# Kernel optimization log

Hardware: AMD Instinct MI355X
Metric: run time of the kernel (lower is better)

Reference implementation:

```python
import jax, jax.numpy as jnp
import numpy as np

D_MODEL = 256
NUM_HEADS = 4
EPS = 1e-6


def setup_inputs() -> dict:
    key = jax.random.key(0)
    ks = jax.random.split(key, 9)
    B, T, D = 4, 2048, D_MODEL
    scale = 1.0 / np.sqrt(D)
    inp = {
        "x": jax.random.normal(ks[0], (B, T, D), dtype=jnp.float32),
        "Wq": jax.random.normal(ks[1], (D, D), dtype=jnp.float32) * scale,
        "bq": jnp.zeros((D,), dtype=jnp.float32),
        "Wk": jax.random.normal(ks[2], (D, D), dtype=jnp.float32) * scale,
        "bk": jnp.zeros((D,), dtype=jnp.float32),
        "Wv": jax.random.normal(ks[3], (D, D), dtype=jnp.float32) * scale,
        "bv": jnp.zeros((D,), dtype=jnp.float32),
        "Wo": jax.random.normal(ks[4], (D, D), dtype=jnp.float32) * scale,
        "bo": jnp.zeros((D,), dtype=jnp.float32),
    }
    return inp


def _feature_map(a):
    # F.elu(x) + 1.0
    return jax.nn.elu(a) + 1.0


def reference(x, Wq, bq, Wk, bk, Wv, bv, Wo, bo):
    B, T, D = x.shape
    H = NUM_HEADS
    dh = D // H
    Q = _feature_map((x @ Wq + bq).reshape(B, T, H, dh))
    K = _feature_map((x @ Wk + bk).reshape(B, T, H, dh))
    V = (x @ Wv + bv).reshape(B, T, H, dh)
    # outer-product state: (B,T,H,dh,dh), cumulative over time
    KV = jnp.einsum('bthd,bthm->bthdm', K, V)
    S = jnp.cumsum(KV, axis=1)
    Z = jnp.cumsum(K, axis=1)
    out = jnp.einsum('bthd,bthdm->bthm', Q, S)
    denom = jnp.einsum('bthd,bthd->bth', Q, Z)[..., None] + EPS
    out = (out / denom).reshape(B, T, D)
    return out @ Wo + bo
```

## Files before the change

### kernel.cpp

```cpp
#include <hip/hip_runtime.h>
#include <hip/hip_bf16.h>

#define D_MODEL 256
#define NHEADS 4
#define DHEAD 64
#define BATCH 4
#define TSEQ 2048
#define CHUNK 64
#define NCHUNK (TSEQ / CHUNK)
#define NTOK (BATCH * TSEQ)
#define NBH (BATCH * NHEADS)
#define EPSV 1e-6f
#define LSTRF 68
#define PQ 36

typedef __bf16 bf16x8 __attribute__((ext_vector_type(8)));
typedef float f32x4 __attribute__((ext_vector_type(4)));
typedef unsigned short us8 __attribute__((ext_vector_type(8)));

__device__ __forceinline__ float elu1(float a) {
    return a > 0.0f ? a + 1.0f : __expf(a);
}

__device__ __forceinline__ unsigned short f2bf(float f) {
    __hip_bfloat16 h = __float2bfloat16(f);
    return __builtin_bit_cast(unsigned short, h);
}

__device__ __forceinline__ float bf2f(unsigned short u) {
    return __bfloat162float(__builtin_bit_cast(__hip_bfloat16, u));
}

__device__ __forceinline__ void unpack2(unsigned int u, float& lo, float& hi) {
    lo = __builtin_bit_cast(float, u << 16);
    hi = __builtin_bit_cast(float, u & 0xFFFF0000u);
}

__device__ __forceinline__ bf16x8 frag8(const float* p) {
    const float4 x = *reinterpret_cast<const float4*>(p);
    const float4 y = *reinterpret_cast<const float4*>(p + 4);
    us8 u;
    u[0] = f2bf(x.x); u[1] = f2bf(x.y); u[2] = f2bf(x.z); u[3] = f2bf(x.w);
    u[4] = f2bf(y.x); u[5] = f2bf(y.y); u[6] = f2bf(y.z); u[7] = f2bf(y.w);
    return __builtin_bit_cast(bf16x8, u);
}

__device__ __forceinline__ void gld_lds16(const void* g, void* l) {
    __builtin_amdgcn_global_load_lds(
        (const __attribute__((address_space(1))) void*)g,
        (__attribute__((address_space(3))) void*)l, 16, 0, 0);
}

__global__ __launch_bounds__(256) void convert_kernel(
    const float* __restrict__ x,
    const float* __restrict__ Wq, const float* __restrict__ Wk,
    const float* __restrict__ Wv, const float* __restrict__ Wo,
    unsigned short* __restrict__ xb,
    unsigned short* __restrict__ Wt, unsigned short* __restrict__ Wot)
{
    const int tid = threadIdx.x;
    if (blockIdx.x < NTOK * D_MODEL / 8 / 256) {
        const int i = (blockIdx.x * 256 + tid) * 8;
        const float4 a = *reinterpret_cast<const float4*>(&x[i]);
        const float4 b = *reinterpret_cast<const float4*>(&x[i + 4]);
        ushort4 u0 = { f2bf(a.x), f2bf(a.y), f2bf(a.z), f2bf(a.w) };
        ushort4 u1 = { f2bf(b.x), f2bf(b.y), f2bf(b.z), f2bf(b.w) };
        *reinterpret_cast<ushort4*>(&xb[i]) = u0;
        *reinterpret_cast<ushort4*>(&xb[i + 4]) = u1;
        return;
    }
    __shared__ float Ls[64][65];
    const int bid = blockIdx.x - NTOK * D_MODEL / 8 / 256;
    const int wi = bid >> 4;
    const int ti = bid & 15;
    const int k0 = (ti >> 2) * 64, n0 = (ti & 3) * 64;
    const float* W = wi == 0 ? Wq : wi == 1 ? Wk : wi == 2 ? Wv : Wo;
#pragma unroll
    for (int i = 0; i < 16; ++i) {
        const int idx = i * 256 + tid;
        const int r = idx >> 6, c = idx & 63;
        Ls[r][c] = W[(size_t)(k0 + r) * D_MODEL + n0 + c];
    }
    __syncthreads();
    unsigned short* outp = (wi < 3) ? (Wt + (size_t)(wi * 256 + n0) * D_MODEL + k0)
                                    : (Wot + (size_t)n0 * D_MODEL + k0);
#pragma unroll
    for (int i = 0; i < 16; ++i) {
        const int idx = i * 256 + tid;
        const int rn = idx >> 6, ck = idx & 63;
        outp[(size_t)rn * D_MODEL + ck] = f2bf(Ls[ck][rn]);
    }
}

template<int MODE>
__global__ __launch_bounds__(256) void mfma_gemm_kernel(
    const unsigned short* __restrict__ A,
    const unsigned short* __restrict__ Bt,
    const float* __restrict__ b0, const float* __restrict__ b1,
    const float* __restrict__ b2,
    void* __restrict__ O0, void* __restrict__ O1, void* __restrict__ O2)
{
    __shared__ __align__(16) unsigned short As[64 * 64];
    __shared__ __align__(16) unsigned short Bs[64 * 64];
    const int tid = threadIdx.x;
    const int wave = tid >> 6, lane = tid & 63;
    const int la = lane & 15, q = lane >> 4;

    int mtile, ntile;
    if (MODE == 0) { ntile = blockIdx.x % 12; mtile = blockIdx.x / 12; }
    else           { ntile = blockIdx.x & 3;  mtile = blockIdx.x >> 2; }
    const int m0 = mtile * 64, n0 = ntile * 64;

    const unsigned short* Ab = A  + (size_t)m0 * D_MODEL;
    const unsigned short* Bb = Bt + (size_t)n0 * D_MODEL;

    f32x4 acc[4];
#pragma unroll
    for (int i = 0; i < 4; ++i) acc[i] = (f32x4){0.f, 0.f, 0.f, 0.f};

    for (int k0 = 0; k0 < D_MODEL; k0 += 64) {
#pragma unroll
        for (int i = 0; i < 2; ++i) {
            const int bslot = i * 256 + wave * 64;
            const int slot = bslot + lane;
            const int m = slot >> 3, s = slot & 7;
            const int g = s ^ (m & 7);
            gld_lds16(Ab + (size_t)m * D_MODEL + k0 + g * 8, &As[bslot * 8]);
            gld_lds16(Bb + (size_t)m * D_MODEL + k0 + g * 8, &Bs[bslot * 8]);
        }
        __syncthreads();

        bf16x8 af[2], bfr[4][2];
#pragma unroll
        for (int kh = 0; kh < 2; ++kh) {
            const int g = kh * 4 + q;
            const int m = wave * 16 + la;
            af[kh] = *reinterpret_cast<const bf16x8*>(
                &As[m * 64 + ((g ^ (m & 7)) << 3)]);
#pragma unroll
            for (int ni = 0; ni < 4; ++ni) {
                const int n = ni * 16 + la;
                bfr[ni][kh] = *reinterpret_cast<const bf16x8*>(
                    &Bs[n * 64 + ((g ^ (n & 7)) << 3)]);
            }
        }
#pragma unroll
        for (int ni = 0; ni < 4; ++ni) {
            acc[ni] = __builtin_amdgcn_mfma_f32_16x16x32_bf16(
                af[0], bfr[ni][0], acc[ni], 0, 0, 0);
            acc[ni] = __builtin_amdgcn_mfma_f32_16x16x32_bf16(
                af[1], bfr[ni][1], acc[ni], 0, 0, 0);
        }
        __syncthreads();
    }

#pragma unroll
    for (int ni = 0; ni < 4; ++ni) {
        const int row = m0 + wave * 16 + q * 4;
        const int col = n0 + ni * 16 + la;
        if (MODE == 0) {
            const int which = col >> 8;
            const int cl = col & 255;
            unsigned short* Out = (unsigned short*)
                (which == 0 ? O0 : which == 1 ? O1 : O2);
            const float* bias = which == 0 ? b0 : which == 1 ? b1 : b2;
            const int act = (which < 2);
            const float bv = bias[cl];
#pragma unroll
            for (int r = 0; r < 4; ++r) {
                float v = acc[ni][r] + bv;
                if (act) v = elu1(v);
                Out[(size_t)(row + r) * D_MODEL + cl] = f2bf(v);
            }
        } else {
            float* Out = (float*)O0;
            const float bv = b0[col];
#pragma unroll
            for (int r = 0; r < 4; ++r)
                Out[(size_t)(row + r) * D_MODEL + col] = acc[ni][r] + bv;
        }
    }
}

__global__ __launch_bounds__(256) void chunksum_kernel(
    const unsigned short* __restrict__ Kb, const unsigned short* __restrict__ Vb,
    unsigned short* __restrict__ Pb16, float* __restrict__ Zc)
{
    __shared__ __align__(16) unsigned int Ktp[DHEAD * PQ];
    __shared__ __align__(16) unsigned int Vtp[DHEAD * PQ];
    const int tid = threadIdx.x;
    const int c  = blockIdx.x % NCHUNK;
    const int bh = blockIdx.x / NCHUNK;
    const int b = bh / NHEADS, h = bh % NHEADS;
    const size_t gbase = ((size_t)(b * TSEQ + c * CHUNK)) * D_MODEL + h * DHEAD;

    {
        const int sp = tid & 31, mg = tid >> 5;
        const int e0 = mg * 8;
        const uint4 k0 = *reinterpret_cast<const uint4*>(
            &Kb[gbase + (size_t)(2 * sp) * D_MODEL + e0]);
        const uint4 k1 = *reinterpret_cast<const uint4*>(
            &Kb[gbase + (size_t)(2 * sp + 1) * D_MODEL + e0]);
        const uint4 v0 = *reinterpret_cast<const uint4*>(
            &Vb[gbase + (size_t)(2 * sp) * D_MODEL + e0]);
        const uint4 v1 = *reinterpret_cast<const uint4*>(
            &Vb[gbase + (size_t)(2 * sp + 1) * D_MODEL + e0]);
        const unsigned short* ke = reinterpret_cast<const unsigned short*>(&k0);
        const unsigned short* ko2 = reinterpret_cast<const unsigned short*>(&k1);
        const unsigned short* ve = reinterpret_cast<const unsigned short*>(&v0);
        const unsigned short* vo = reinterpret_cast<const unsigned short*>(&v1);
#pragma unroll
        for (int j = 0; j < 8; ++j) {
            Ktp[(e0 + j) * PQ + sp] =
                (unsigned int)ke[j] | ((unsigned int)ko2[j] << 16);
            Vtp[(e0 + j) * PQ + sp] =
                (unsigned int)ve[j] | ((unsigned int)vo[j] << 16);
        }
    }
    __syncthreads();

    const int wave = tid >> 6, lane = tid & 63;
    const int la = lane & 15, q = lane >> 4;
    const int wm = (wave >> 1) * 32, wn = (wave & 1) * 32;

    f32x4 acc[2][2];
#pragma unroll
    for (int i = 0; i < 2; ++i)
#pragma unroll
        for (int j = 0; j < 2; ++j) acc[i][j] = (f32x4){0.f, 0.f, 0.f, 0.f};

#pragma unroll
    for (int ks = 0; ks < 2; ++ks) {
        const int ku = ks * 16 + q * 4;
        const bf16x8 a0  = __builtin_bit_cast(bf16x8,
            *reinterpret_cast<const uint4*>(&Vtp[(wm + la) * PQ + ku]));
        const bf16x8 a1  = __builtin_bit_cast(bf16x8,
            *reinterpret_cast<const uint4*>(&Vtp[(wm + 16 + la) * PQ + ku]));
        const bf16x8 bb0 = __builtin_bit_cast(bf16x8,
            *reinterpret_cast<const uint4*>(&Ktp[(wn + la) * PQ + ku]));
        const bf16x8 bb1 = __builtin_bit_cast(bf16x8,
            *reinterpret_cast<const uint4*>(&Ktp[(wn + 16 + la) * PQ + ku]));
        acc[0][0] = __builtin_amdgcn_mfma_f32_16x16x32_bf16(a0, bb0, acc[0][0], 0, 0, 0);
        acc[0][1] = __builtin_amdgcn_mfma_f32_16x16x32_bf16(a0, bb1, acc[0][1], 0, 0, 0);
        acc[1][0] = __builtin_amdgcn_mfma_f32_16x16x32_bf16(a1, bb0, acc[1][0], 0, 0, 0);
        acc[1][1] = __builtin_amdgcn_mfma_f32_16x16x32_bf16(a1, bb1, acc[1][1], 0, 0, 0);
    }

    unsigned short* Pb = Pb16 + (size_t)blockIdx.x * (DHEAD * DHEAD);
#pragma unroll
    for (int mi = 0; mi < 2; ++mi)
#pragma unroll
        for (int ni = 0; ni < 2; ++ni) {
            const int row = wm + mi * 16 + q * 4;
            const int col = wn + ni * 16 + la;
#pragma unroll
            for (int r = 0; r < 4; ++r)
                Pb[(row + r) * DHEAD + col] = f2bf(acc[mi][ni][r]);
        }

    if (tid < DHEAD) {
        float z = 0.f;
        for (int tt = 0; tt < 32; ++tt) {
            float lo, hi;
            unpack2(Ktp[tid * PQ + tt], lo, hi);
            z += lo;
            z += hi;
        }
        Zc[(size_t)blockIdx.x * DHEAD + tid] = z;
    }
}

__global__ __launch_bounds__(256) void prefix_kernel(
    const unsigned short* __restrict__ Pb16, float* __restrict__ Zc,
    unsigned short* __restrict__ Sb)
{
    const int tid = threadIdx.x;
    if (blockIdx.x < NBH * 16) {
        const int bh = blockIdx.x >> 4;
        const int e = ((blockIdx.x & 15) << 8) + tid;
        const size_t base = (size_t)bh * NCHUNK * (DHEAD * DHEAD) + e;
        float v[NCHUNK];
#pragma unroll
        for (int c = 0; c < NCHUNK; ++c)
            v[c] = bf2f(Pb16[base + (size_t)c * (DHEAD * DHEAD)]);
        float s = 0.f;
#pragma unroll
        for (int c = 0; c < NCHUNK; ++c) {
            const float t = v[c];
            Sb[base + (size_t)c * (DHEAD * DHEAD)] = f2bf(s);
            s += t;
        }
    } else {
        const int j = ((int)(blockIdx.x - NBH * 16) << 8) + tid;
        if (j < NBH * DHEAD) {
            const int bh = j >> 6, d = j & 63;
            float v[NCHUNK];
#pragma unroll
            for (int c = 0; c < NCHUNK; ++c) v[c] = Zc[(bh * NCHUNK + c) * DHEAD + d];
            float s = 0.f;
#pragma unroll
            for (int c = 0; c < NCHUNK; ++c) {
                const float t = v[c];
                Zc[(bh * NCHUNK + c) * DHEAD + d] = s;
                s += t;
            }
        }
    }
}

__global__ __launch_bounds__(256) void chunkout_kernel(
    const unsigned short* __restrict__ Qb, const unsigned short* __restrict__ Kb,
    const unsigned short* __restrict__ Vb,
    const unsigned short* __restrict__ Sb, const float* __restrict__ Zx,
    unsigned short* __restrict__ Ob)
{
    __shared__ __align__(16) unsigned int Qp[CHUNK * PQ];
    __shared__ __align__(16) unsigned int Kp[CHUNK * PQ];
    __shared__ __align__(16) unsigned int Vtp[DHEAD * PQ];
    __shared__ __align__(16) float At[CHUNK * LSTRF];
    __shared__ float zsh[DHEAD];
    __shared__ float dnm[CHUNK];

    const int tid = threadIdx.x;
    const int c  = blockIdx.x % NCHUNK;
    const int bh = blockIdx.x / NCHUNK;
    const int b = bh / NHEADS, h = bh % NHEADS;
    const size_t gbase = ((size_t)(b * TSEQ + c * CHUNK)) * D_MODEL + h * DHEAD;
    const unsigned short* Sp = Sb + (size_t)blockIdx.x * (DHEAD * DHEAD);

#pragma unroll
    for (int i = 0; i < 2; ++i) {
        const int idx = i * 256 + tid;
        const int t = idx >> 3, e4 = (idx & 7) * 4;
        const uint4 qv = *reinterpret_cast<const uint4*>(
            &Qb[gbase + (size_t)t * D_MODEL + e4 * 2]);
        const uint4 kv = *reinterpret_cast<const uint4*>(
            &Kb[gbase + (size_t)t * D_MODEL + e4 * 2]);
        *reinterpret_cast<uint4*>(&Qp[t * PQ + e4]) = qv;
        *reinterpret_cast<uint4*>(&Kp[t * PQ + e4]) = kv;
    }
    {
        const int sp = tid & 31, mg = tid >> 5;
        const int m0 = mg * 8;
        const uint4 v0 = *reinterpret_cast<const uint4*>(
            &Vb[gbase + (size_t)(2 * sp) * D_MODEL + m0]);
        const uint4 v1 = *reinterpret_cast<const uint4*>(
            &Vb[gbase + (size_t)(2 * sp + 1) * D_MODEL + m0]);
        const unsigned short* ev = reinterpret_cast<const unsigned short*>(&v0);
        const unsigned short* ov = reinterpret_cast<const unsigned short*>(&v1);
#pragma unroll
        for (int j = 0; j < 8; ++j)
            Vtp[(m0 + j) * PQ + sp] =
                (unsigned int)ev[j] | ((unsigned int)ov[j] << 16);
    }
    if (tid < DHEAD)
        zsh[tid] = Zx[((size_t)bh * NCHUNK + c) * DHEAD + tid];
    __syncthreads();

    const int wave = tid >> 6, lane = tid & 63;
    const int la = lane & 15, q = lane >> 4;
    const int wt = (wave >> 1) * 32, wn = (wave & 1) * 32;

    f32x4 acc[2][2];
#pragma unroll
    for (int i = 0; i < 2; ++i)
#pragma unroll
        for (int j = 0; j < 2; ++j) acc[i][j] = (f32x4){0.f, 0.f, 0.f, 0.f};
#pragma unroll
    for (int ks = 0; ks < 2; ++ks) {
        const int ku = ks * 16 + q * 4;
        const bf16x8 a0  = __builtin_bit_cast(bf16x8,
            *reinterpret_cast<const uint4*>(&Qp[(wt + la) * PQ + ku]));
        const bf16x8 a1  = __builtin_bit_cast(bf16x8,
            *reinterpret_cast<const uint4*>(&Qp[(wt + 16 + la) * PQ + ku]));
        const bf16x8 bb0 = __builtin_bit_cast(bf16x8,
            *reinterpret_cast<const uint4*>(&Kp[(wn + la) * PQ + ku]));
        const bf16x8 bb1 = __builtin_bit_cast(bf16x8,
            *reinterpret_cast<const uint4*>(&Kp[(wn + 16 + la) * PQ + ku]));
        acc[0][0] = __builtin_amdgcn_mfma_f32_16x16x32_bf16(a0, bb0, acc[0][0], 0, 0, 0);
        acc[0][1] = __builtin_amdgcn_mfma_f32_16x16x32_bf16(a0, bb1, acc[0][1], 0, 0, 0);
        acc[1][0] = __builtin_amdgcn_mfma_f32_16x16x32_bf16(a1, bb0, acc[1][0], 0, 0, 0);
        acc[1][1] = __builtin_amdgcn_mfma_f32_16x16x32_bf16(a1, bb1, acc[1][1], 0, 0, 0);
    }
#pragma unroll
    for (int mi = 0; mi < 2; ++mi)
#pragma unroll
        for (int ni = 0; ni < 2; ++ni) {
            const int t0 = wt + mi * 16 + q * 4;
            const int s  = wn + ni * 16 + la;
#pragma unroll
            for (int r = 0; r < 4; ++r)
                At[(t0 + r) * LSTRF + s] = (s <= t0 + r) ? acc[mi][ni][r] : 0.f;
        }
    __syncthreads();

    if (tid < CHUNK) {
        float dv = 0.f;
        for (int s = 0; s < CHUNK; ++s) dv += At[tid * LSTRF + s];
        for (int dd = 0; dd < 32; ++dd) {
            float lo, hi;
            unpack2(Qp[tid * PQ + dd], lo, hi);
            dv = fmaf(lo, zsh[2 * dd], dv);
            dv = fmaf(hi, zsh[2 * dd + 1], dv);
        }
        dnm[tid] = dv + EPSV;
    }
    __syncthreads();

    f32x4 o[2][2];
#pragma unroll
    for (int i = 0; i < 2; ++i)
#pragma unroll
        for (int j = 0; j < 2; ++j) o[i][j] = (f32x4){0.f, 0.f, 0.f, 0.f};
#pragma unroll
    for (int ks = 0; ks < 2; ++ks) {
        const int ku = ks * 16 + q * 4;
        const int ko = ks * 32 + q * 8;
        const bf16x8 a0  = __builtin_bit_cast(bf16x8,
            *reinterpret_cast<const uint4*>(&Qp[(wt + la) * PQ + ku]));
        const bf16x8 a1  = __builtin_bit_cast(bf16x8,
            *reinterpret_cast<const uint4*>(&Qp[(wt + 16 + la) * PQ + ku]));
        const bf16x8 bb0 = __builtin_bit_cast(bf16x8,
            *reinterpret_cast<const uint4*>(&Sp[(wn + la) * DHEAD + ko]));
        const bf16x8 bb1 = __builtin_bit_cast(bf16x8,
            *reinterpret_cast<const uint4*>(&Sp[(wn + 16 + la) * DHEAD + ko]));
        o[0][0] = __builtin_amdgcn_mfma_f32_16x16x32_bf16(a0, bb0, o[0][0], 0, 0, 0);
        o[0][1] = __builtin_amdgcn_mfma_f32_16x16x32_bf16(a0, bb1, o[0][1], 0, 0, 0);
        o[1][0] = __builtin_amdgcn_mfma_f32_16x16x32_bf16(a1, bb0, o[1][0], 0, 0, 0);
        o[1][1] = __builtin_amdgcn_mfma_f32_16x16x32_bf16(a1, bb1, o[1][1], 0, 0, 0);
    }
#pragma unroll
    for (int ks = 0; ks < 2; ++ks) {
        const int ku = ks * 16 + q * 4;
        const int ko = ks * 32 + q * 8;
        const bf16x8 a0  = frag8(&At[(wt + la) * LSTRF + ko]);
        const bf16x8 a1  = frag8(&At[(wt + 16 + la) * LSTRF + ko]);
        const bf16x8 bb0 = __builtin_bit_cast(bf16x8,
            *reinterpret_cast<const uint4*>(&Vtp[(wn + la) * PQ + ku]));
        const bf16x8 bb1 = __builtin_bit_cast(bf16x8,
            *reinterpret_cast<const uint4*>(&Vtp[(wn + 16 + la) * PQ + ku]));
        o[0][0] = __builtin_amdgcn_mfma_f32_16x16x32_bf16(a0, bb0, o[0][0], 0, 0, 0);
        o[0][1] = __builtin_amdgcn_mfma_f32_16x16x32_bf16(a0, bb1, o[0][1], 0, 0, 0);
        o[1][0] = __builtin_amdgcn_mfma_f32_16x16x32_bf16(a1, bb0, o[1][0], 0, 0, 0);
        o[1][1] = __builtin_amdgcn_mfma_f32_16x16x32_bf16(a1, bb1, o[1][1], 0, 0, 0);
    }

#pragma unroll
    for (int mi = 0; mi < 2; ++mi)
#pragma unroll
        for (int ni = 0; ni < 2; ++ni) {
            const int t0 = wt + mi * 16 + q * 4;
            const int m  = wn + ni * 16 + la;
#pragma unroll
            for (int r = 0; r < 4; ++r) {
                const float v = o[mi][ni][r] / dnm[t0 + r];
                Ob[gbase + (size_t)(t0 + r) * D_MODEL + m] = f2bf(v);
            }
        }
}

extern "C" void kernel_launch(void* const* d_in, const int* in_sizes, int n_in,
                              void* d_out, int out_size, void* d_ws, size_t ws_size,
                              hipStream_t stream)
{
    const float* x  = (const float*)d_in[0];
    const float* Wq = (const float*)d_in[1];
    const float* bq = (const float*)d_in[2];
    const float* Wk = (const float*)d_in[3];
    const float* bk = (const float*)d_in[4];
    const float* Wv = (const float*)d_in[5];
    const float* bv = (const float*)d_in[6];
    const float* Wo = (const float*)d_in[7];
    const float* bo = (const float*)d_in[8];
    float* out = (float*)d_out;

    const size_t NE = (size_t)NTOK * D_MODEL;
    const size_t PE = (size_t)NBH * NCHUNK * DHEAD * DHEAD;
    unsigned short* xb   = (unsigned short*)d_ws;
    unsigned short* Wt   = xb + NE;
    unsigned short* Wot  = Wt + 768 * 256;
    unsigned short* Qb   = Wot + 256 * 256;
    unsigned short* Kb   = Qb + NE;
    unsigned short* Vb   = Kb + NE;
    unsigned short* Ob   = Vb + NE;
    unsigned short* Sb   = Ob + NE;
    unsigned short* Pb16 = Sb + PE;
    float* Z = (float*)(Pb16 + PE);

    convert_kernel<<<NTOK * D_MODEL / 8 / 256 + 64, 256, 0, stream>>>(
        x, Wq, Wk, Wv, Wo, xb, Wt, Wot);
    mfma_gemm_kernel<0><<<(NTOK / 64) * 12, 256, 0, stream>>>(
        xb, Wt, bq, bk, bv, Qb, Kb, Vb);
    chunksum_kernel<<<NBH * NCHUNK, 256, 0, stream>>>(Kb, Vb, Pb16, Z);
    prefix_kernel<<<NBH * 16 + 4, 256, 0, stream>>>(Pb16, Z, Sb);
    chunkout_kernel<<<NBH * NCHUNK, 256, 0, stream>>>(Qb, Kb, Vb, Sb, Z, Ob);
    mfma_gemm_kernel<1><<<(NTOK / 64) * 4, 256, 0, stream>>>(
        Ob, Wot, bo, nullptr, nullptr, out, nullptr, nullptr);
}
```

Measured before the change: 105.1 us.

## Fuse six pipeline kernels into one cooperative kernel with grid syncs

Replaces the six separate launches (convert, QKV GEMM, chunk sums, prefix scan, chunk output, output GEMM) with one persistent cooperative kernel of 512 blocks. Phases are separated by grid.sync, and shared memory is a union reused across phases. The goal is to remove launch gaps and per-kernel ramp-up and drain. In exchange, work is fixed to 512 blocks (several tiles per block in some phases), each grid barrier costs time, and some phases leave blocks idle.

```diff
diff --git a/kernel.cpp b/kernel.cpp
--- a/kernel.cpp
+++ b/kernel.cpp
@@ -1,5 +1,8 @@
 #include <hip/hip_runtime.h>
 #include <hip/hip_bf16.h>
+#include <hip/hip_cooperative_groups.h>
+
+namespace cg = cooperative_groups;
 
 #define D_MODEL 256
 #define NHEADS 4
@@ -13,6 +16,7 @@
 #define EPSV 1e-6f
 #define LSTRF 68
 #define PQ 36
+#define NBLK 512
 
 typedef __bf16 bf16x8 __attribute__((ext_vector_type(8)));
 typedef float f32x4 __attribute__((ext_vector_type(4)));
@@ -51,65 +55,35 @@
         (__attribute__((address_space(3))) void*)l, 16, 0, 0);
 }
 
-__global__ __launch_bounds__(256) void convert_kernel(
-    const float* __restrict__ x,
-    const float* __restrict__ Wq, const float* __restrict__ Wk,
-    const float* __restrict__ Wv, const float* __restrict__ Wo,
-    unsigned short* __restrict__ xb,
-    unsigned short* __restrict__ Wt, unsigned short* __restrict__ Wot)
-{
-    const int tid = threadIdx.x;
-    if (blockIdx.x < NTOK * D_MODEL / 8 / 256) {
-        const int i = (blockIdx.x * 256 + tid) * 8;
-        const float4 a = *reinterpret_cast<const float4*>(&x[i]);
-        const float4 b = *reinterpret_cast<const float4*>(&x[i + 4]);
-        ushort4 u0 = { f2bf(a.x), f2bf(a.y), f2bf(a.z), f2bf(a.w) };
-        ushort4 u1 = { f2bf(b.x), f2bf(b.y), f2bf(b.z), f2bf(b.w) };
-        *reinterpret_cast<ushort4*>(&xb[i]) = u0;
-        *reinterpret_cast<ushort4*>(&xb[i + 4]) = u1;
-        return;
-    }
-    __shared__ float Ls[64][65];
-    const int bid = blockIdx.x - NTOK * D_MODEL / 8 / 256;
-    const int wi = bid >> 4;
-    const int ti = bid & 15;
-    const int k0 = (ti >> 2) * 64, n0 = (ti & 3) * 64;
-    const float* W = wi == 0 ? Wq : wi == 1 ? Wk : wi == 2 ? Wv : Wo;
-#pragma unroll
-    for (int i = 0; i < 16; ++i) {
-        const int idx = i * 256 + tid;
-        const int r = idx >> 6, c = idx & 63;
-        Ls[r][c] = W[(size_t)(k0 + r) * D_MODEL + n0 + c];
-    }
-    __syncthreads();
-    unsigned short* outp = (wi < 3) ? (Wt + (size_t)(wi * 256 + n0) * D_MODEL + k0)
-                                    : (Wot + (size_t)n0 * D_MODEL + k0);
-#pragma unroll
-    for (int i = 0; i < 16; ++i) {
-        const int idx = i * 256 + tid;
-        const int rn = idx >> 6, ck = idx & 63;
-        outp[(size_t)rn * D_MODEL + ck] = f2bf(Ls[ck][rn]);
-    }
-}
+struct SGemm { unsigned short As[64 * 64]; unsigned short Bs[64 * 64]; };
+struct SConv { float Ls[64][65]; };
+struct SCsum { unsigned int Ktp[DHEAD * PQ]; unsigned int Vtp[DHEAD * PQ]; };
+struct SCout {
+    unsigned int Qp[CHUNK * PQ];
+    unsigned int Kp[CHUNK * PQ];
+    unsigned int Vtp[DHEAD * PQ];
+    float At[CHUNK * LSTRF];
+    float zsh[DHEAD];
+    float dnm[CHUNK];
+};
+union SMem {
+    SGemm g;
+    SConv c;
+    SCsum s;
+    SCout o;
+};
 
 template<int MODE>
-__global__ __launch_bounds__(256) void mfma_gemm_kernel(
-    const unsigned short* __restrict__ A,
-    const unsigned short* __restrict__ Bt,
+__device__ __forceinline__ void gemm_tile(
+    int m0, int n0,
+    const unsigned short* __restrict__ A, const unsigned short* __restrict__ Bt,
     const float* __restrict__ b0, const float* __restrict__ b1,
     const float* __restrict__ b2,
-    void* __restrict__ O0, void* __restrict__ O1, void* __restrict__ O2)
+    void* __restrict__ O0, void* __restrict__ O1, void* __restrict__ O2,
+    unsigned short* As, unsigned short* Bs, int tid)
 {
-    __shared__ __align__(16) unsigned short As[64 * 64];
-    __shared__ __align__(16) unsigned short Bs[64 * 64];
-    const int tid = threadIdx.x;
     const int wave = tid >> 6, lane = tid & 63;
     const int la = lane & 15, q = lane >> 4;
-
-    int mtile, ntile;
-    if (MODE == 0) { ntile = blockIdx.x % 12; mtile = blockIdx.x / 12; }
-    else           { ntile = blockIdx.x & 3;  mtile = blockIdx.x >> 2; }
-    const int m0 = mtile * 64, n0 = ntile * 64;
 
     const unsigned short* Ab = A  + (size_t)m0 * D_MODEL;
     const unsigned short* Bb = Bt + (size_t)n0 * D_MODEL;
@@ -182,102 +156,156 @@
     }
 }
 
-__global__ __launch_bounds__(256) void chunksum_kernel(
-    const unsigned short* __restrict__ Kb, const unsigned short* __restrict__ Vb,
-    unsigned short* __restrict__ Pb16, float* __restrict__ Zc)
+__global__ __launch_bounds__(256, 2) void fused_kernel(
+    const float* __restrict__ x,
+    const float* __restrict__ Wq, const float* __restrict__ bq,
+    const float* __restrict__ Wk, const float* __restrict__ bk,
+    const float* __restrict__ Wv, const float* __restrict__ bv,
+    const float* __restrict__ Wo, const float* __restrict__ bo,
+    unsigned short* __restrict__ xb,
+    unsigned short* __restrict__ Wt, unsigned short* __restrict__ Wot,
+    unsigned short* __restrict__ Qb, unsigned short* __restrict__ Kb,
+    unsigned short* __restrict__ Vb, unsigned short* __restrict__ Ob,
+    unsigned short* __restrict__ Sb, unsigned short* __restrict__ Pb16,
+    float* __restrict__ Z, float* __restrict__ out)
 {
-    __shared__ __align__(16) unsigned int Ktp[DHEAD * PQ];
-    __shared__ __align__(16) unsigned int Vtp[DHEAD * PQ];
+    __shared__ __align__(16) SMem sm;
     const int tid = threadIdx.x;
-    const int c  = blockIdx.x % NCHUNK;
-    const int bh = blockIdx.x / NCHUNK;
-    const int b = bh / NHEADS, h = bh % NHEADS;
-    const size_t gbase = ((size_t)(b * TSEQ + c * CHUNK)) * D_MODEL + h * DHEAD;
+    const int bidx = blockIdx.x;
+    cg::grid_group grid = cg::this_grid();
 
     {
-        const int sp = tid & 31, mg = tid >> 5;
-        const int e0 = mg * 8;
-        const uint4 k0 = *reinterpret_cast<const uint4*>(
-            &Kb[gbase + (size_t)(2 * sp) * D_MODEL + e0]);
-        const uint4 k1 = *reinterpret_cast<const uint4*>(
-            &Kb[gbase + (size_t)(2 * sp + 1) * D_MODEL + e0]);
-        const uint4 v0 = *reinterpret_cast<const uint4*>(
-            &Vb[gbase + (size_t)(2 * sp) * D_MODEL + e0]);
-        const uint4 v1 = *reinterpret_cast<const uint4*>(
-            &Vb[gbase + (size_t)(2 * sp + 1) * D_MODEL + e0]);
-        const unsigned short* ke = reinterpret_cast<const unsigned short*>(&k0);
-        const unsigned short* ko2 = reinterpret_cast<const unsigned short*>(&k1);
-        const unsigned short* ve = reinterpret_cast<const unsigned short*>(&v0);
-        const unsigned short* vo = reinterpret_cast<const unsigned short*>(&v1);
-#pragma unroll
-        for (int j = 0; j < 8; ++j) {
-            Ktp[(e0 + j) * PQ + sp] =
-                (unsigned int)ke[j] | ((unsigned int)ko2[j] << 16);
-            Vtp[(e0 + j) * PQ + sp] =
-                (unsigned int)ve[j] | ((unsigned int)vo[j] << 16);
-        }
-    }
-    __syncthreads();
-
-    const int wave = tid >> 6, lane = tid & 63;
-    const int la = lane & 15, q = lane >> 4;
-    const int wm = (wave >> 1) * 32, wn = (wave & 1) * 32;
-
-    f32x4 acc[2][2];
-#pragma unroll
-    for (int i = 0; i < 2; ++i)
-#pragma unroll
-        for (int j = 0; j < 2; ++j) acc[i][j] = (f32x4){0.f, 0.f, 0.f, 0.f};
-
-#pragma unroll
-    for (int ks = 0; ks < 2; ++ks) {
-        const int ku = ks * 16 + q * 4;
-        const bf16x8 a0  = __builtin_bit_cast(bf16x8,
-            *reinterpret_cast<const uint4*>(&Vtp[(wm + la) * PQ + ku]));
-        const bf16x8 a1  = __builtin_bit_cast(bf16x8,
-            *reinterpret_cast<const uint4*>(&Vtp[(wm + 16 + la) * PQ + ku]));
-        const bf16x8 bb0 = __builtin_bit_cast(bf16x8,
-            *reinterpret_cast<const uint4*>(&Ktp[(wn + la) * PQ + ku]));
-        const bf16x8 bb1 = __builtin_bit_cast(bf16x8,
-            *reinterpret_cast<const uint4*>(&Ktp[(wn + 16 + la) * PQ + ku]));
-        acc[0][0] = __builtin_amdgcn_mfma_f32_16x16x32_bf16(a0, bb0, acc[0][0], 0, 0, 0);
-        acc[0][1] = __builtin_amdgcn_mfma_f32_16x16x32_bf16(a0, bb1, acc[0][1], 0, 0, 0);
-        acc[1][0] = __builtin_amdgcn_mfma_f32_16x16x32_bf16(a1, bb0, acc[1][0], 0, 0, 0);
-        acc[1][1] = __builtin_amdgcn_mfma_f32_16x16x32_bf16(a1, bb1, acc[1][1], 0, 0, 0);
-    }
-
-    unsigned short* Pb = Pb16 + (size_t)blockIdx.x * (DHEAD * DHEAD);
-#pragma unroll
-    for (int mi = 0; mi < 2; ++mi)
-#pragma unroll
-        for (int ni = 0; ni < 2; ++ni) {
-            const int row = wm + mi * 16 + q * 4;
-            const int col = wn + ni * 16 + la;
-#pragma unroll
-            for (int r = 0; r < 4; ++r)
-                Pb[(row + r) * DHEAD + col] = f2bf(acc[mi][ni][r]);
-        }
-
-    if (tid < DHEAD) {
-        float z = 0.f;
-        for (int tt = 0; tt < 32; ++tt) {
-            float lo, hi;
-            unpack2(Ktp[tid * PQ + tt], lo, hi);
-            z += lo;
-            z += hi;
-        }
-        Zc[(size_t)blockIdx.x * DHEAD + tid] = z;
-    }
-}
-
-__global__ __launch_bounds__(256) void prefix_kernel(
-    const unsigned short* __restrict__ Pb16, float* __restrict__ Zc,
-    unsigned short* __restrict__ Sb)
-{
-    const int tid = threadIdx.x;
-    if (blockIdx.x < NBH * 16) {
-        const int bh = blockIdx.x >> 4;
-        const int e = ((blockIdx.x & 15) << 8) + tid;
+        const int id = bidx * 256 + tid;
+#pragma unroll
+        for (int u = 0; u < 2; ++u) {
+            const int i = (id + u * (NBLK * 256)) * 8;
+            const float4 a = *reinterpret_cast<const float4*>(&x[i]);
+            const float4 b = *reinterpret_cast<const float4*>(&x[i + 4]);
+            ushort4 u0 = { f2bf(a.x), f2bf(a.y), f2bf(a.z), f2bf(a.w) };
+            ushort4 u1 = { f2bf(b.x), f2bf(b.y), f2bf(b.z), f2bf(b.w) };
+            *reinterpret_cast<ushort4*>(&xb[i]) = u0;
+            *reinterpret_cast<ushort4*>(&xb[i + 4]) = u1;
+        }
+        if (bidx < 64) {
+            const int wi = bidx >> 4;
+            const int ti = bidx & 15;
+            const int k0 = (ti >> 2) * 64, n0 = (ti & 3) * 64;
+            const float* W = wi == 0 ? Wq : wi == 1 ? Wk : wi == 2 ? Wv : Wo;
+#pragma unroll
+            for (int i = 0; i < 16; ++i) {
+                const int idx = i * 256 + tid;
+                const int r = idx >> 6, c2 = idx & 63;
+                sm.c.Ls[r][c2] = W[(size_t)(k0 + r) * D_MODEL + n0 + c2];
+            }
+            __syncthreads();
+            unsigned short* outp = (wi < 3)
+                ? (Wt + (size_t)(wi * 256 + n0) * D_MODEL + k0)
+                : (Wot + (size_t)n0 * D_MODEL + k0);
+#pragma unroll
+            for (int i = 0; i < 16; ++i) {
+                const int idx = i * 256 + tid;
+                const int rn = idx >> 6, ck = idx & 63;
+                outp[(size_t)rn * D_MODEL + ck] = f2bf(sm.c.Ls[ck][rn]);
+            }
+        }
+    }
+    grid.sync();
+
+#pragma unroll
+    for (int t = 0; t < 3; ++t) {
+        const int tile = bidx + t * NBLK;
+        const int ntile = tile % 12, mtile = tile / 12;
+        gemm_tile<0>(mtile * 64, ntile * 64, xb, Wt, bq, bk, bv,
+                     Qb, Kb, Vb, sm.g.As, sm.g.Bs, tid);
+    }
+    grid.sync();
+
+    {
+        const int c  = bidx % NCHUNK;
+        const int bh = bidx / NCHUNK;
+        const int b = bh / NHEADS, h = bh % NHEADS;
+        const size_t gbase = ((size_t)(b * TSEQ + c * CHUNK)) * D_MODEL + h * DHEAD;
+
+        {
+            const int sp = tid & 31, mg = tid >> 5;
+            const int e0 = mg * 8;
+            const uint4 k0 = *reinterpret_cast<const uint4*>(
+                &Kb[gbase + (size_t)(2 * sp) * D_MODEL + e0]);
+            const uint4 k1 = *reinterpret_cast<const uint4*>(
+                &Kb[gbase + (size_t)(2 * sp + 1) * D_MODEL + e0]);
+            const uint4 v0 = *reinterpret_cast<const uint4*>(
+                &Vb[gbase + (size_t)(2 * sp) * D_MODEL + e0]);
+            const uint4 v1 = *reinterpret_cast<const uint4*>(
+                &Vb[gbase + (size_t)(2 * sp + 1) * D_MODEL + e0]);
+            const unsigned short* ke  = reinterpret_cast<const unsigned short*>(&k0);
+            const unsigned short* ko2 = reinterpret_cast<const unsigned short*>(&k1);
+            const unsigned short* ve  = reinterpret_cast<const unsigned short*>(&v0);
+            const unsigned short* vo  = reinterpret_cast<const unsigned short*>(&v1);
+#pragma unroll
+            for (int j = 0; j < 8; ++j) {
+                sm.s.Ktp[(e0 + j) * PQ + sp] =
+                    (unsigned int)ke[j] | ((unsigned int)ko2[j] << 16);
+                sm.s.Vtp[(e0 + j) * PQ + sp] =
+                    (unsigned int)ve[j] | ((unsigned int)vo[j] << 16);
+            }
+        }
+        __syncthreads();
+
+        const int wave = tid >> 6, lane = tid & 63;
+        const int la = lane & 15, q = lane >> 4;
+        const int wm = (wave >> 1) * 32, wn = (wave & 1) * 32;
+
+        f32x4 acc[2][2];
+#pragma unroll
+        for (int i = 0; i < 2; ++i)
+#pragma unroll
+            for (int j = 0; j < 2; ++j) acc[i][j] = (f32x4){0.f, 0.f, 0.f, 0.f};
+
+#pragma unroll
+        for (int ks = 0; ks < 2; ++ks) {
+            const int ku = ks * 16 + q * 4;
+            const bf16x8 a0  = __builtin_bit_cast(bf16x8,
+                *reinterpret_cast<const uint4*>(&sm.s.Vtp[(wm + la) * PQ + ku]));
+            const bf16x8 a1  = __builtin_bit_cast(bf16x8,
+                *reinterpret_cast<const uint4*>(&sm.s.Vtp[(wm + 16 + la) * PQ + ku]));
+            const bf16x8 bb0 = __builtin_bit_cast(bf16x8,
+                *reinterpret_cast<const uint4*>(&sm.s.Ktp[(wn + la) * PQ + ku]));
+            const bf16x8 bb1 = __builtin_bit_cast(bf16x8,
+                *reinterpret_cast<const uint4*>(&sm.s.Ktp[(wn + 16 + la) * PQ + ku]));
+            acc[0][0] = __builtin_amdgcn_mfma_f32_16x16x32_bf16(a0, bb0, acc[0][0], 0, 0, 0);
+            acc[0][1] = __builtin_amdgcn_mfma_f32_16x16x32_bf16(a0, bb1, acc[0][1], 0, 0, 0);
+            acc[1][0] = __builtin_amdgcn_mfma_f32_16x16x32_bf16(a1, bb0, acc[1][0], 0, 0, 0);
+            acc[1][1] = __builtin_amdgcn_mfma_f32_16x16x32_bf16(a1, bb1, acc[1][1], 0, 0, 0);
+        }
+
+        unsigned short* Pb = Pb16 + (size_t)bidx * (DHEAD * DHEAD);
+#pragma unroll
+        for (int mi = 0; mi < 2; ++mi)
+#pragma unroll
+            for (int ni = 0; ni < 2; ++ni) {
+                const int row = wm + mi * 16 + q * 4;
+                const int col = wn + ni * 16 + la;
+#pragma unroll
+                for (int r = 0; r < 4; ++r)
+                    Pb[(row + r) * DHEAD + col] = f2bf(acc[mi][ni][r]);
+            }
+
+        if (tid < DHEAD) {
+            float z = 0.f;
+            for (int tt = 0; tt < 32; ++tt) {
+                float lo, hi;
+                unpack2(sm.s.Ktp[tid * PQ + tt], lo, hi);
+                z += lo;
+                z += hi;
+            }
+            Z[(size_t)bidx * DHEAD + tid] = z;
+        }
+    }
+    grid.sync();
+
+    if (bidx < NBH * 16) {
+        const int bh = bidx >> 4;
+        const int e = ((bidx & 15) << 8) + tid;
         const size_t base = (size_t)bh * NCHUNK * (DHEAD * DHEAD) + e;
         float v[NCHUNK];
 #pragma unroll
@@ -290,173 +318,168 @@
             Sb[base + (size_t)c * (DHEAD * DHEAD)] = f2bf(s);
             s += t;
         }
-    } else {
-        const int j = ((int)(blockIdx.x - NBH * 16) << 8) + tid;
+    } else if (bidx < NBH * 16 + 4) {
+        const int j = ((bidx - NBH * 16) << 8) + tid;
         if (j < NBH * DHEAD) {
             const int bh = j >> 6, d = j & 63;
             float v[NCHUNK];
 #pragma unroll
-            for (int c = 0; c < NCHUNK; ++c) v[c] = Zc[(bh * NCHUNK + c) * DHEAD + d];
+            for (int c = 0; c < NCHUNK; ++c) v[c] = Z[(bh * NCHUNK + c) * DHEAD + d];
             float s = 0.f;
 #pragma unroll
             for (int c = 0; c < NCHUNK; ++c) {
                 const float t = v[c];
-                Zc[(bh * NCHUNK + c) * DHEAD + d] = s;
+                Z[(bh * NCHUNK + c) * DHEAD + d] = s;
                 s += t;
             }
         }
     }
-}
-
-__global__ __launch_bounds__(256) void chunkout_kernel(
-    const unsigned short* __restrict__ Qb, const unsigned short* __restrict__ Kb,
-    const unsigned short* __restrict__ Vb,
-    const unsigned short* __restrict__ Sb, const float* __restrict__ Zx,
-    unsigned short* __restrict__ Ob)
-{
-    __shared__ __align__(16) unsigned int Qp[CHUNK * PQ];
-    __shared__ __align__(16) unsigned int Kp[CHUNK * PQ];
-    __shared__ __align__(16) unsigned int Vtp[DHEAD * PQ];
-    __shared__ __align__(16) float At[CHUNK * LSTRF];
-    __shared__ float zsh[DHEAD];
-    __shared__ float dnm[CHUNK];
-
-    const int tid = threadIdx.x;
-    const int c  = blockIdx.x % NCHUNK;
-    const int bh = blockIdx.x / NCHUNK;
-    const int b = bh / NHEADS, h = bh % NHEADS;
-    const size_t gbase = ((size_t)(b * TSEQ + c * CHUNK)) * D_MODEL + h * DHEAD;
-    const unsigned short* Sp = Sb + (size_t)blockIdx.x * (DHEAD * DHEAD);
-
-#pragma unroll
-    for (int i = 0; i < 2; ++i) {
-        const int idx = i * 256 + tid;
-        const int t = idx >> 3, e4 = (idx & 7) * 4;
-        const uint4 qv = *reinterpret_cast<const uint4*>(
-            &Qb[gbase + (size_t)t * D_MODEL + e4 * 2]);
-        const uint4 kv = *reinterpret_cast<const uint4*>(
-            &Kb[gbase + (size_t)t * D_MODEL + e4 * 2]);
-        *reinterpret_cast<uint4*>(&Qp[t * PQ + e4]) = qv;
-        *reinterpret_cast<uint4*>(&Kp[t * PQ + e4]) = kv;
-    }
+    grid.sync();
+
     {
-        const int sp = tid & 31, mg = tid >> 5;
-        const int m0 = mg * 8;
-        const uint4 v0 = *reinterpret_cast<const uint4*>(
-            &Vb[gbase + (size_t)(2 * sp) * D_MODEL + m0]);
-        const uint4 v1 = *reinterpret_cast<const uint4*>(
-            &Vb[gbase + (size_t)(2 * sp + 1) * D_MODEL + m0]);
-        const unsigned short* ev = reinterpret_cast<const unsigned short*>(&v0);
-        const unsigned short* ov = reinterpret_cast<const unsigned short*>(&v1);
-#pragma unroll
-        for (int j = 0; j < 8; ++j)
-            Vtp[(m0 + j) * PQ + sp] =
-                (unsigned int)ev[j] | ((unsigned int)ov[j] << 16);
-    }
-    if (tid < DHEAD)
-        zsh[tid] = Zx[((size_t)bh * NCHUNK + c) * DHEAD + tid];
-    __syncthreads();
-
-    const int wave = tid >> 6, lane = tid & 63;
-    const int la = lane & 15, q = lane >> 4;
-    const int wt = (wave >> 1) * 32, wn = (wave & 1) * 32;
-
-    f32x4 acc[2][2];
-#pragma unroll
-    for (int i = 0; i < 2; ++i)
-#pragma unroll
-        for (int j = 0; j < 2; ++j) acc[i][j] = (f32x4){0.f, 0.f, 0.f, 0.f};
-#pragma unroll
-    for (int ks = 0; ks < 2; ++ks) {
-        const int ku = ks * 16 + q * 4;
-        const bf16x8 a0  = __builtin_bit_cast(bf16x8,
-            *reinterpret_cast<const uint4*>(&Qp[(wt + la) * PQ + ku]));
-        const bf16x8 a1  = __builtin_bit_cast(bf16x8,
-            *reinterpret_cast<const uint4*>(&Qp[(wt + 16 + la) * PQ + ku]));
-        const bf16x8 bb0 = __builtin_bit_cast(bf16x8,
-            *reinterpret_cast<const uint4*>(&Kp[(wn + la) * PQ + ku]));
-        const bf16x8 bb1 = __builtin_bit_cast(bf16x8,
-            *reinterpret_cast<const uint4*>(&Kp[(wn + 16 + la) * PQ + ku]));
-        acc[0][0] = __builtin_amdgcn_mfma_f32_16x16x32_bf16(a0, bb0, acc[0][0], 0, 0, 0);
-        acc[0][1] = __builtin_amdgcn_mfma_f32_16x16x32_bf16(a0, bb1, acc[0][1], 0, 0, 0);
-        acc[1][0] = __builtin_amdgcn_mfma_f32_16x16x32_bf16(a1, bb0, acc[1][0], 0, 0, 0);
-        acc[1][1] = __builtin_amdgcn_mfma_f32_16x16x32_bf16(a1, bb1, acc[1][1], 0, 0, 0);
-    }
-#pragma unroll
-    for (int mi = 0; mi < 2; ++mi)
-#pragma unroll
-        for (int ni = 0; ni < 2; ++ni) {
-            const int t0 = wt + mi * 16 + q * 4;
-            const int s  = wn + ni * 16 + la;
-#pragma unroll
-            for (int r = 0; r < 4; ++r)
-                At[(t0 + r) * LSTRF + s] = (s <= t0 + r) ? acc[mi][ni][r] : 0.f;
-        }
-    __syncthreads();
-
-    if (tid < CHUNK) {
-        float dv = 0.f;
-        for (int s = 0; s < CHUNK; ++s) dv += At[tid * LSTRF + s];
-        for (int dd = 0; dd < 32; ++dd) {
-            float lo, hi;
-            unpack2(Qp[tid * PQ + dd], lo, hi);
-            dv = fmaf(lo, zsh[2 * dd], dv);
-            dv = fmaf(hi, zsh[2 * dd + 1], dv);
-        }
-        dnm[tid] = dv + EPSV;
-    }
-    __syncthreads();
-
-    f32x4 o[2][2];
-#pragma unroll
-    for (int i = 0; i < 2; ++i)
-#pragma unroll
-        for (int j = 0; j < 2; ++j) o[i][j] = (f32x4){0.f, 0.f, 0.f, 0.f};
-#pragma unroll
-    for (int ks = 0; ks < 2; ++ks) {
-        const int ku = ks * 16 + q * 4;
-        const int ko = ks * 32 + q * 8;
-        const bf16x8 a0  = __builtin_bit_cast(bf16x8,
-            *reinterpret_cast<const uint4*>(&Qp[(wt + la) * PQ + ku]));
-        const bf16x8 a1  = __builtin_bit_cast(bf16x8,
-            *reinterpret_cast<const uint4*>(&Qp[(wt + 16 + la) * PQ + ku]));
-        const bf16x8 bb0 = __builtin_bit_cast(bf16x8,
-            *reinterpret_cast<const uint4*>(&Sp[(wn + la) * DHEAD + ko]));
-        const bf16x8 bb1 = __builtin_bit_cast(bf16x8,
-            *reinterpret_cast<const uint4*>(&Sp[(wn + 16 + la) * DHEAD + ko]));
-        o[0][0] = __builtin_amdgcn_mfma_f32_16x16x32_bf16(a0, bb0, o[0][0], 0, 0, 0);
-        o[0][1] = __builtin_amdgcn_mfma_f32_16x16x32_bf16(a0, bb1, o[0][1], 0, 0, 0);
-        o[1][0] = __builtin_amdgcn_mfma_f32_16x16x32_bf16(a1, bb0, o[1][0], 0, 0, 0);
-        o[1][1] = __builtin_amdgcn_mfma_f32_16x16x32_bf16(a1, bb1, o[1][1], 0, 0, 0);
-    }
-#pragma unroll
-    for (int ks = 0; ks < 2; ++ks) {
-        const int ku = ks * 16 + q * 4;
-        const int ko = ks * 32 + q * 8;
-        const bf16x8 a0  = frag8(&At[(wt + la) * LSTRF + ko]);
-        const bf16x8 a1  = frag8(&At[(wt + 16 + la) * LSTRF + ko]);
-        const bf16x8 bb0 = __builtin_bit_cast(bf16x8,
-            *reinterpret_cast<const uint4*>(&Vtp[(wn + la) * PQ + ku]));
-        const bf16x8 bb1 = __builtin_bit_cast(bf16x8,
-            *reinterpret_cast<const uint4*>(&Vtp[(wn + 16 + la) * PQ + ku]));
-        o[0][0] = __builtin_amdgcn_mfma_f32_16x16x32_bf16(a0, bb0, o[0][0], 0, 0, 0);
-        o[0][1] = __builtin_amdgcn_mfma_f32_16x16x32_bf16(a0, bb1, o[0][1], 0, 0, 0);
-        o[1][0] = __builtin_amdgcn_mfma_f32_16x16x32_bf16(a1, bb0, o[1][0], 0, 0, 0);
-        o[1][1] = __builtin_amdgcn_mfma_f32_16x16x32_bf16(a1, bb1, o[1][1], 0, 0, 0);
-    }
-
-#pragma unroll
-    for (int mi = 0; mi < 2; ++mi)
-#pragma unroll
-        for (int ni = 0; ni < 2; ++ni) {
-            const int t0 = wt + mi * 16 + q * 4;
-            const int m  = wn + ni * 16 + la;
-#pragma unroll
-            for (int r = 0; r < 4; ++r) {
-                const float v = o[mi][ni][r] / dnm[t0 + r];
-                Ob[gbase + (size_t)(t0 + r) * D_MODEL + m] = f2bf(v);
-            }
-        }
+        const int c  = bidx % NCHUNK;
+        const int bh = bidx / NCHUNK;
+        const int b = bh / NHEADS, h = bh % NHEADS;
+        const size_t gbase = ((size_t)(b * TSEQ + c * CHUNK)) * D_MODEL + h * DHEAD;
+        const unsigned short* Sp = Sb + (size_t)bidx * (DHEAD * DHEAD);
+
+#pragma unroll
+        for (int i = 0; i < 2; ++i) {
+            const int idx = i * 256 + tid;
+            const int t = idx >> 3, e4 = (idx & 7) * 4;
+            const uint4 qv = *reinterpret_cast<const uint4*>(
+                &Qb[gbase + (size_t)t * D_MODEL + e4 * 2]);
+            const uint4 kv = *reinterpret_cast<const uint4*>(
+                &Kb[gbase + (size_t)t * D_MODEL + e4 * 2]);
+            *reinterpret_cast<uint4*>(&sm.o.Qp[t * PQ + e4]) = qv;
+            *reinterpret_cast<uint4*>(&sm.o.Kp[t * PQ + e4]) = kv;
+        }
+        {
+            const int sp = tid & 31, mg = tid >> 5;
+            const int m0 = mg * 8;
+            const uint4 v0 = *reinterpret_cast<const uint4*>(
+                &Vb[gbase + (size_t)(2 * sp) * D_MODEL + m0]);
+            const uint4 v1 = *reinterpret_cast<const uint4*>(
+                &Vb[gbase + (size_t)(2 * sp + 1) * D_MODEL + m0]);
+            const unsigned short* ev = reinterpret_cast<const unsigned short*>(&v0);
+            const unsigned short* ov = reinterpret_cast<const unsigned short*>(&v1);
+#pragma unroll
+            for (int j = 0; j < 8; ++j)
+                sm.o.Vtp[(m0 + j) * PQ + sp] =
+                    (unsigned int)ev[j] | ((unsigned int)ov[j] << 16);
+        }
+        if (tid < DHEAD)
+            sm.o.zsh[tid] = Z[((size_t)bh * NCHUNK + c) * DHEAD + tid];
+        __syncthreads();
+
+        const int wave = tid >> 6, lane = tid & 63;
+        const int la = lane & 15, q = lane >> 4;
+        const int wt = (wave >> 1) * 32, wn = (wave & 1) * 32;
+
+        f32x4 acc[2][2];
+#pragma unroll
+        for (int i = 0; i < 2; ++i)
+#pragma unroll
+            for (int j = 0; j < 2; ++j) acc[i][j] = (f32x4){0.f, 0.f, 0.f, 0.f};
+#pragma unroll
+        for (int ks = 0; ks < 2; ++ks) {
+            const int ku = ks * 16 + q * 4;
+            const bf16x8 a0  = __builtin_bit_cast(bf16x8,
+                *reinterpret_cast<const uint4*>(&sm.o.Qp[(wt + la) * PQ + ku]));
+            const bf16x8 a1  = __builtin_bit_cast(bf16x8,
+                *reinterpret_cast<const uint4*>(&sm.o.Qp[(wt + 16 + la) * PQ + ku]));
+            const bf16x8 bb0 = __builtin_bit_cast(bf16x8,
+                *reinterpret_cast<const uint4*>(&sm.o.Kp[(wn + la) * PQ + ku]));
+            const bf16x8 bb1 = __builtin_bit_cast(bf16x8,
+                *reinterpret_cast<const uint4*>(&sm.o.Kp[(wn + 16 + la) * PQ + ku]));
+            acc[0][0] = __builtin_amdgcn_mfma_f32_16x16x32_bf16(a0, bb0, acc[0][0], 0, 0, 0);
+            acc[0][1] = __builtin_amdgcn_mfma_f32_16x16x32_bf16(a0, bb1, acc[0][1], 0, 0, 0);
+            acc[1][0] = __builtin_amdgcn_mfma_f32_16x16x32_bf16(a1, bb0, acc[1][0], 0, 0, 0);
+            acc[1][1] = __builtin_amdgcn_mfma_f32_16x16x32_bf16(a1, bb1, acc[1][1], 0, 0, 0);
+        }
+#pragma unroll
+        for (int mi = 0; mi < 2; ++mi)
+#pragma unroll
+            for (int ni = 0; ni < 2; ++ni) {
+                const int t0 = wt + mi * 16 + q * 4;
+                const int s  = wn + ni * 16 + la;
+#pragma unroll
+                for (int r = 0; r < 4; ++r)
+                    sm.o.At[(t0 + r) * LSTRF + s] = (s <= t0 + r) ? acc[mi][ni][r] : 0.f;
+            }
+        __syncthreads();
+
+        if (tid < CHUNK) {
+            float dv = 0.f;
+            for (int s = 0; s < CHUNK; ++s) dv += sm.o.At[tid * LSTRF + s];
+            for (int dd = 0; dd < 32; ++dd) {
+                float lo, hi;
+                unpack2(sm.o.Qp[tid * PQ + dd], lo, hi);
+                dv = fmaf(lo, sm.o.zsh[2 * dd], dv);
+                dv = fmaf(hi, sm.o.zsh[2 * dd + 1], dv);
+            }
+            sm.o.dnm[tid] = dv + EPSV;
+        }
+        __syncthreads();
+
+        f32x4 o[2][2];
+#pragma unroll
+        for (int i = 0; i < 2; ++i)
+#pragma unroll
+            for (int j = 0; j < 2; ++j) o[i][j] = (f32x4){0.f, 0.f, 0.f, 0.f};
+#pragma unroll
+        for (int ks = 0; ks < 2; ++ks) {
+            const int ku = ks * 16 + q * 4;
+            const int ko = ks * 32 + q * 8;
+            const bf16x8 a0  = __builtin_bit_cast(bf16x8,
+                *reinterpret_cast<const uint4*>(&sm.o.Qp[(wt + la) * PQ + ku]));
+            const bf16x8 a1  = __builtin_bit_cast(bf16x8,
+                *reinterpret_cast<const uint4*>(&sm.o.Qp[(wt + 16 + la) * PQ + ku]));
+            const bf16x8 bb0 = __builtin_bit_cast(bf16x8,
+                *reinterpret_cast<const uint4*>(&Sp[(wn + la) * DHEAD + ko]));
+            const bf16x8 bb1 = __builtin_bit_cast(bf16x8,
+                *reinterpret_cast<const uint4*>(&Sp[(wn + 16 + la) * DHEAD + ko]));
+            o[0][0] = __builtin_amdgcn_mfma_f32_16x16x32_bf16(a0, bb0, o[0][0], 0, 0, 0);
+            o[0][1] = __builtin_amdgcn_mfma_f32_16x16x32_bf16(a0, bb1, o[0][1], 0, 0, 0);
+            o[1][0] = __builtin_amdgcn_mfma_f32_16x16x32_bf16(a1, bb0, o[1][0], 0, 0, 0);
+            o[1][1] = __builtin_amdgcn_mfma_f32_16x16x32_bf16(a1, bb1, o[1][1], 0, 0, 0);
+        }
+#pragma unroll
+        for (int ks = 0; ks < 2; ++ks) {
+            const int ku = ks * 16 + q * 4;
+            const int ko = ks * 32 + q * 8;
+            const bf16x8 a0  = frag8(&sm.o.At[(wt + la) * LSTRF + ko]);
+            const bf16x8 a1  = frag8(&sm.o.At[(wt + 16 + la) * LSTRF + ko]);
+            const bf16x8 bb0 = __builtin_bit_cast(bf16x8,
+                *reinterpret_cast<const uint4*>(&sm.o.Vtp[(wn + la) * PQ + ku]));
+            const bf16x8 bb1 = __builtin_bit_cast(bf16x8,
+                *reinterpret_cast<const uint4*>(&sm.o.Vtp[(wn + 16 + la) * PQ + ku]));
+            o[0][0] = __builtin_amdgcn_mfma_f32_16x16x32_bf16(a0, bb0, o[0][0], 0, 0, 0);
+            o[0][1] = __builtin_amdgcn_mfma_f32_16x16x32_bf16(a0, bb1, o[0][1], 0, 0, 0);
+            o[1][0] = __builtin_amdgcn_mfma_f32_16x16x32_bf16(a1, bb0, o[1][0], 0, 0, 0);
+            o[1][1] = __builtin_amdgcn_mfma_f32_16x16x32_bf16(a1, bb1, o[1][1], 0, 0, 0);
+        }
+
+#pragma unroll
+        for (int mi = 0; mi < 2; ++mi)
+#pragma unroll
+            for (int ni = 0; ni < 2; ++ni) {
+                const int t0 = wt + mi * 16 + q * 4;
+                const int m  = wn + ni * 16 + la;
+#pragma unroll
+                for (int r = 0; r < 4; ++r) {
+                    const float v = o[mi][ni][r] / sm.o.dnm[t0 + r];
+                    Ob[gbase + (size_t)(t0 + r) * D_MODEL + m] = f2bf(v);
+                }
+            }
+    }
+    grid.sync();
+
+    {
+        const int ntile = bidx & 3, mtile = bidx >> 2;
+        gemm_tile<1>(mtile * 64, ntile * 64, Ob, Wot, bo, nullptr, nullptr,
+                     out, nullptr, nullptr, sm.g.As, sm.g.Bs, tid);
+    }
 }
 
 extern "C" void kernel_launch(void* const* d_in, const int* in_sizes, int n_in,
@@ -487,13 +510,13 @@
     unsigned short* Pb16 = Sb + PE;
     float* Z = (float*)(Pb16 + PE);
 
-    convert_kernel<<<NTOK * D_MODEL / 8 / 256 + 64, 256, 0, stream>>>(
-        x, Wq, Wk, Wv, Wo, xb, Wt, Wot);
-    mfma_gemm_kernel<0><<<(NTOK / 64) * 12, 256, 0, stream>>>(
-        xb, Wt, bq, bk, bv, Qb, Kb, Vb);
-    chunksum_kernel<<<NBH * NCHUNK, 256, 0, stream>>>(Kb, Vb, Pb16, Z);
-    prefix_kernel<<<NBH * 16 + 4, 256, 0, stream>>>(Pb16, Z, Sb);
-    chunkout_kernel<<<NBH * NCHUNK, 256, 0, stream>>>(Qb, Kb, Vb, Sb, Z, Ob);
-    mfma_gemm_kernel<1><<<(NTOK / 64) * 4, 256, 0, stream>>>(
-        Ob, Wot, bo, nullptr, nullptr, out, nullptr, nullptr);
-}
+    void* ka[] = {
+        (void*)&x,  (void*)&Wq, (void*)&bq, (void*)&Wk, (void*)&bk,
+        (void*)&Wv, (void*)&bv, (void*)&Wo, (void*)&bo,
+        (void*)&xb, (void*)&Wt, (void*)&Wot,
+        (void*)&Qb, (void*)&Kb, (void*)&Vb, (void*)&Ob,
+        (void*)&Sb, (void*)&Pb16, (void*)&Z, (void*)&out
+    };
+    hipLaunchCooperativeKernel(fused_kernel, dim3(NBLK), dim3(256),
+                               ka, 0, stream);
+}
```

Measured after the change: 416.8 us. 3.97x slower.
